# Kernel optimization log

Measured on AMD Instinct MI355X. Metric: run time of the kernel, lower is better.

## Reference

```python
import jax, jax.numpy as jnp
import numpy as np

B, L, E, H = 8, 1024, 512, 8
E2 = 2 * E
EPS = 1e-5


def _spectral_fc(x, w, fw, fb, n):
    # rfft along feature dim, multiply by rfft of learned filter w (1,n), irfft back, then Linear
    xf = jnp.fft.rfft(x, axis=2, norm='ortho')          # [B,L,n//2+1] complex
    wf = jnp.fft.rfft(w, axis=1, norm='ortho')          # [1,n//2+1] complex
    y = jnp.fft.irfft(xf * wf, n=n, axis=2, norm='ortho')
    return y @ fw + fb


def _layernorm(x, g, b):
    m = jnp.mean(x, axis=-1, keepdims=True)
    v = jnp.mean(jnp.square(x - m), axis=-1, keepdims=True)
    return (x - m) * jax.lax.rsqrt(v + EPS) * g + b


def setup_inputs() -> dict:
    key = jax.random.key(0)
    ks = jax.random.split(key, 32)
    s = 0.02

    def lin_w(k, i, o):
        return (jax.random.normal(k, (i, o), jnp.float32) / np.sqrt(i)).astype(jnp.float32)

    def layer_params(k0, k1, n):
        return (s * jax.random.normal(k0, (1, n), jnp.float32), lin_w(k1, n, n), jnp.zeros((n,), jnp.float32))

    attn_w, attn_fw, attn_fb = layer_params(ks[1], ks[2], E)
    ln0_w, ln0_fw, ln0_fb = layer_params(ks[3], ks[4], E)
    ln1_w, ln1_fw, ln1_fb = layer_params(ks[5], ks[6], E)
    ln2_w, ln2_fw, ln2_fb = layer_params(ks[7], ks[8], E)
    ln3_w, ln3_fw, ln3_fb = layer_params(ks[9], ks[10], E2)
    ln4_w, ln4_fw, ln4_fb = layer_params(ks[11], ks[12], E2)

    return {
        'x': jax.random.normal(ks[0], (B, L, E), jnp.float32),
        'attn_w': attn_w, 'attn_fw': attn_fw, 'attn_fb': attn_fb,
        'ln0_w': ln0_w, 'ln0_fw': ln0_fw, 'ln0_fb': ln0_fb,
        'ln1_w': ln1_w, 'ln1_fw': ln1_fw, 'ln1_fb': ln1_fb,
        'ln2_w': ln2_w, 'ln2_fw': ln2_fw, 'ln2_fb': ln2_fb,
        'ln3_w': ln3_w, 'ln3_fw': ln3_fw, 'ln3_fb': ln3_fb,
        'ln4_w': ln4_w, 'ln4_fw': ln4_fw, 'ln4_fb': ln4_fb,
        'n1_g': jnp.ones((E,), jnp.float32), 'n1_b': jnp.zeros((E,), jnp.float32),
        'n2_g': jnp.ones((E,), jnp.float32), 'n2_b': jnp.zeros((E,), jnp.float32),
    }


def reference(x, attn_w, attn_fw, attn_fb,
              ln0_w, ln0_fw, ln0_fb, ln1_w, ln1_fw, ln1_fb,
              ln2_w, ln2_fw, ln2_fb, ln3_w, ln3_fw, ln3_fb,
              ln4_w, ln4_fw, ln4_fb, n1_g, n1_b, n2_g, n2_b):
    q = _spectral_fc(x, attn_w, attn_fw, attn_fb, E).reshape(B, L, H, E // H)
    scores = jnp.einsum('blhe,bshe->bhls', q, q) * (1.0 / np.sqrt(E))
    A = jax.nn.softmax(scores, axis=-1)
    new_x = jnp.einsum('bhls,bshd->blhd', A, q).reshape(B, L, E)

    x1 = _layernorm(x + new_x, n1_g, n1_b)
    x_ln = jax.nn.gelu(_spectral_fc(x1, ln0_w, ln0_fw, ln0_fb, E), approximate=False)
    x2 = x1 - x_ln
    h = jax.nn.sigmoid(_spectral_fc(x2, ln1_w, ln1_fw, ln1_fb, E)) * _spectral_fc(x2, ln2_w, ln2_fw, ln2_fb, E)
    out = jnp.concatenate((new_x, x_ln), axis=-1)  # [B,L,2E]
    out = jax.nn.sigmoid(_spectral_fc(out, ln3_w, ln3_fw, ln3_fb, E2)) * _spectral_fc(out, ln4_w, ln4_fw, ln4_fb, E2)
    return (_layernorm(h, n2_g, n2_b), out)
```

## Files before the change

kernel.cpp:

```cpp
#include <hip/hip_runtime.h>
#include <hip/hip_bf16.h>
#include <math.h>

typedef __hip_bfloat16 bf16;
typedef unsigned short u16;
typedef __attribute__((ext_vector_type(8))) short short8;
typedef __attribute__((ext_vector_type(4))) float f32x4;

#define NB      8
#define SEQ     1024
#define EDIM    512
#define E2DIM   1024
#define ROWS    8192
#define INV_SQRT_E 0.04419417382415922f
#define ATT_SCL    0.06375985678148161f

__device__ inline u16 f2bu(float f) {
    union { float f; unsigned u; } c; c.f = f;
    return (u16)((c.u + 0x7FFF + ((c.u >> 16) & 1)) >> 16);
}

__device__ __forceinline__ unsigned cvtpk_bf16(float lo, float hi) {
    unsigned r;
    asm("v_cvt_pk_bf16_f32 %0, %1, %2" : "=v"(r) : "v"(lo), "v"(hi));
    return r;
}

__global__ __launch_bounds__(256) void detect_dtype(const u16* __restrict__ x,
                                                    int* __restrict__ flag) {
    int t = threadIdx.x;
    int cnt = 0;
    for (int k = t; k < 8192; k += 256) {
        int e = (x[k] >> 7) & 0xFF;
        if (e >= 0xC0) cnt++;
    }
#pragma unroll
    for (int o = 32; o > 0; o >>= 1) cnt += __shfl_xor(cnt, o);
    __shared__ int red[4];
    if ((t & 63) == 0) red[t >> 6] = cnt;
    __syncthreads();
    if (t == 0) flag[0] = (red[0] + red[1] + red[2] + red[3] > 100) ? 1 : 0;
}

struct CvtBatch {
    const void* src[23];
    float4*     dst[23];
    int         pre4[24];
};

__global__ __launch_bounds__(256) void cvt_all(CvtBatch a, int total4,
                                               const int* __restrict__ flag) {
    int t = blockIdx.x * 256 + threadIdx.x;
    if (t >= total4) return;
    int lo = 0;
    while (t >= a.pre4[lo + 1]) lo++;
    int li = t - a.pre4[lo];
    if (flag[0]) {
        a.dst[lo][li] = ((const float4*)a.src[lo])[li];
    } else {
        ushort4 u = ((const ushort4*)a.src[lo])[li];
        union { unsigned int i; float f; } c;
        float4 o;
        c.i = ((unsigned)u.x) << 16; o.x = c.f;
        c.i = ((unsigned)u.y) << 16; o.y = c.f;
        c.i = ((unsigned)u.z) << 16; o.z = c.f;
        c.i = ((unsigned)u.w) << 16; o.w = c.f;
        a.dst[lo][li] = o;
    }
}

__global__ __launch_bounds__(256) void f2b_kernel(const float* __restrict__ src,
                                                  u16* __restrict__ dst, int n4) {
    int i = blockIdx.x * 256 + threadIdx.x;
    if (i >= n4) return;
    float4 a = ((const float4*)src)[i];
    ushort4 o;
    o.x = f2bu(a.x); o.y = f2bu(a.y); o.z = f2bu(a.z); o.w = f2bu(a.w);
    ((ushort4*)dst)[i] = o;
}

#define LDK 32

__device__ __forceinline__ void stage128x32(const u16* g, int ld, u16* lds, int tid) {
    const int w = tid >> 6;
    const int l = tid & 63;
    const int r = w * 16 + (l >> 2);
    const int c = (l & 3) * 8;
    const u16* g0 = g + (size_t)r * ld + c;
    u16* l0 = lds + w * 16 * LDK;
    __builtin_amdgcn_global_load_lds(
        (const __attribute__((address_space(1))) void*)g0,
        (__attribute__((address_space(3))) void*)l0, 16, 0, 0);
    const u16* g1 = g0 + (size_t)64 * ld;
    u16* l1 = l0 + 64 * LDK;
    __builtin_amdgcn_global_load_lds(
        (const __attribute__((address_space(1))) void*)g1,
        (__attribute__((address_space(3))) void*)l1, 16, 0, 0);
}

__device__ __forceinline__ void stage64x32(const u16* g, int ld, u16* lds, int tid) {
    const int w = tid >> 6;
    const int l = tid & 63;
    const int r = w * 16 + (l >> 2);
    const int c = (l & 3) * 8;
    const u16* g0 = g + (size_t)r * ld + c;
    u16* l0 = lds + w * 16 * LDK;
    __builtin_amdgcn_global_load_lds(
        (const __attribute__((address_space(1))) void*)g0,
        (__attribute__((address_space(3))) void*)l0, 16, 0, 0);
}

__device__ __forceinline__ void xcd_swz(int& bx, int& by) {
    const int nx  = gridDim.x;
    const int nwg = nx * gridDim.y;
    const int lid = blockIdx.y * nx + blockIdx.x;
    const int q   = nwg >> 3;
    const int s   = (lid & 7) * q + (lid >> 3);
    bx = s % nx;
    by = s / nx;
}

struct FoldBatch {
    const float* w[6];
    const float* fw[6];
    u16* t1[6];
    u16* t2[6];
    u16* mt[6];
    int  n[6], lg[6];
    float sc[6];
};

__global__ __launch_bounds__(256) void fold_trconv(FoldBatch fb) {
    const int z = blockIdx.z;
    const int n = fb.n[z];
    const int bx = blockIdx.x * 32, by = blockIdx.y * 32;
    if (bx >= n || by >= n) return;
    __shared__ float t[32][33];
    const int tx = threadIdx.x & 31, ty = threadIdx.x >> 5;
    const float* src = fb.fw[z];
    u16* dst = fb.t1[z];
#pragma unroll
    for (int r = 0; r < 32; r += 8)
        t[ty + r][tx] = src[(size_t)(by + ty + r) * n + bx + tx];
    __syncthreads();
#pragma unroll
    for (int r = 0; r < 32; r += 8)
        dst[(size_t)(bx + ty + r) * n + by + tx] = f2bu(t[tx][ty + r]);
}

__global__ __launch_bounds__(256) void fold_circ(FoldBatch fb) {
    const int z = blockIdx.z;
    const int n = fb.n[z], lg = fb.lg[z];
    int idx = blockIdx.x * 256 + threadIdx.x;
    if (idx >= n * n) return;
    int mask = n - 1;
    int m = idx & mask;
    int j = idx >> lg;
    fb.t2[z][idx] = f2bu(fb.w[z][(m - j) & mask]);
}

__global__ __launch_bounds__(256) void fold_gemm(FoldBatch fb) {
    const int z = blockIdx.z;
    const int n = fb.n[z];
    const int bm = blockIdx.y * 128, bn = blockIdx.x * 128;
    if (bm >= n || bn >= n) return;
    const u16* A  = fb.t1[z];
    const u16* Bt = fb.t2[z];
    u16* Mt = fb.mt[z];
    const float scale = fb.sc[z];

    __shared__ u16 Asl[2][128 * LDK];
    __shared__ u16 Bsl[2][128 * LDK];
    const int tid = threadIdx.x;
    const int lane = tid & 63, wave = tid >> 6;
    const int wy = wave >> 1, wx = wave & 1;
    const int qd = lane >> 4, ln16 = lane & 15;

    f32x4 acc[4][4];
#pragma unroll
    for (int i = 0; i < 4; i++)
#pragma unroll
        for (int j = 0; j < 4; j++)
#pragma unroll
            for (int r = 0; r < 4; r++) acc[i][j][r] = 0.f;

    const u16* Ab = A  + (size_t)bm * n;
    const u16* Bb = Bt + (size_t)bn * n;
    stage128x32(Ab, n, Asl[0], tid);
    stage128x32(Bb, n, Bsl[0], tid);
    __syncthreads();
    int cur = 0;
    for (int k0 = 0; k0 < n; k0 += 32) {
        if (k0 + 32 < n) {
            stage128x32(Ab + k0 + 32, n, Asl[cur ^ 1], tid);
            stage128x32(Bb + k0 + 32, n, Bsl[cur ^ 1], tid);
        }
        const u16* Ac = Asl[cur];
        const u16* Bc = Bsl[cur];
        short8 af[4], bf_[4];
#pragma unroll
        for (int i = 0; i < 4; i++) {
            af[i]  = *(const short8*)&Ac[(wy * 64 + i * 16 + ln16) * LDK + qd * 8];
            bf_[i] = *(const short8*)&Bc[(wx * 64 + i * 16 + ln16) * LDK + qd * 8];
        }
#pragma unroll
        for (int i = 0; i < 4; i++)
#pragma unroll
            for (int j = 0; j < 4; j++)
                acc[i][j] = __builtin_amdgcn_mfma_f32_16x16x32_bf16(af[i], bf_[j], acc[i][j], 0, 0, 0);
        __syncthreads();
        cur ^= 1;
    }
#pragma unroll
    for (int i = 0; i < 4; i++)
#pragma unroll
        for (int j = 0; j < 4; j++) {
            const int col = bn + wx * 64 + j * 16 + ln16;
#pragma unroll
            for (int r = 0; r < 4; r++) {
                const int row = bm + wy * 64 + i * 16 + qd * 4 + r;
                Mt[(size_t)row * n + col] = f2bu(acc[i][j][r] * scale);
            }
        }
}

__global__ __launch_bounds__(256) void gemm_bf(
    const u16* __restrict__ A, int lda,
    const u16* __restrict__ Bt, int ldb,
    const float* __restrict__ bias,
    float* __restrict__ Cf, int ldc,
    u16* __restrict__ Cb, int ldcb,
    u16* __restrict__ Cb2, int ldcb2,
    const float* __restrict__ aux, int ldaux,
    int K, int mode)
{
    __shared__ u16 Asl[2][128 * LDK];
    __shared__ u16 Bsl[2][64 * LDK];
    const int tid = threadIdx.x;
    int bxs, bys;
    xcd_swz(bxs, bys);
    const int bm = bys * 128, bn = bxs * 64;
    const int lane = tid & 63, wave = tid >> 6;
    const int wy = wave >> 1, wx = wave & 1;
    const int qd = lane >> 4, ln16 = lane & 15;

    f32x4 acc[4][2];
#pragma unroll
    for (int i = 0; i < 4; i++)
#pragma unroll
        for (int j = 0; j < 2; j++)
#pragma unroll
            for (int r = 0; r < 4; r++) acc[i][j][r] = 0.f;

    const u16* Ab = A  + (size_t)bm * lda;
    const u16* Bb = Bt + (size_t)bn * ldb;
    stage128x32(Ab, lda, Asl[0], tid);
    stage64x32(Bb, ldb, Bsl[0], tid);
    __syncthreads();
    int cur = 0;
    for (int k0 = 0; k0 < K; k0 += 32) {
        if (k0 + 32 < K) {
            stage128x32(Ab + k0 + 32, lda, Asl[cur ^ 1], tid);
            stage64x32(Bb + k0 + 32, ldb, Bsl[cur ^ 1], tid);
        }
        const u16* Ac = Asl[cur];
        const u16* Bc = Bsl[cur];
        short8 af[4], bf_[2];
#pragma unroll
        for (int i = 0; i < 4; i++)
            af[i]  = *(const short8*)&Ac[(wy * 64 + i * 16 + ln16) * LDK + qd * 8];
#pragma unroll
        for (int j = 0; j < 2; j++)
            bf_[j] = *(const short8*)&Bc[(wx * 32 + j * 16 + ln16) * LDK + qd * 8];
#pragma unroll
        for (int i = 0; i < 4; i++)
#pragma unroll
            for (int j = 0; j < 2; j++)
                acc[i][j] = __builtin_amdgcn_mfma_f32_16x16x32_bf16(af[i], bf_[j], acc[i][j], 0, 0, 0);
        __syncthreads();
        cur ^= 1;
    }

#pragma unroll
    for (int i = 0; i < 4; i++) {
#pragma unroll
        for (int j = 0; j < 2; j++) {
            const int col = bn + wx * 32 + j * 16 + ln16;
            const float b_ = bias ? bias[col] : 0.f;
#pragma unroll
            for (int r = 0; r < 4; r++) {
                const int row = bm + wy * 64 + i * 16 + qd * 4 + r;
                float v = acc[i][j][r] + b_;
                if (mode == 1) v = 0.5f * v * (1.0f + erff(v * 0.7071067811865476f));
                if (Cf)  Cf[(size_t)row * ldc + col] = v;
                if (Cb)  Cb[(size_t)row * ldcb + col] = f2bu(v);
                if (Cb2) Cb2[(size_t)row * ldcb2 + col] =
                             f2bu(aux[(size_t)row * ldaux + col] - v);
            }
        }
    }
}

__global__ __launch_bounds__(256) void gemm_bf2(
    const u16* __restrict__ A, int lda,
    const u16* __restrict__ B1t, const u16* __restrict__ B2t, int ldb,
    const float* __restrict__ bias1, const float* __restrict__ bias2,
    float* __restrict__ Cf, int ldc, int K)
{
    __shared__ u16 Asl[2][128 * LDK];
    __shared__ u16 B1sl[2][64 * LDK];
    __shared__ u16 B2sl[2][64 * LDK];
    const int tid = threadIdx.x;
    int bxs, bys;
    xcd_swz(bxs, bys);
    const int bm = bys * 128, bn = bxs * 64;
    const int lane = tid & 63, wave = tid >> 6;
    const int wy = wave >> 1, wx = wave & 1;
    const int qd = lane >> 4, ln16 = lane & 15;

    f32x4 acc1[4][2], acc2[4][2];
#pragma unroll
    for (int i = 0; i < 4; i++)
#pragma unroll
        for (int j = 0; j < 2; j++)
#pragma unroll
            for (int r = 0; r < 4; r++) { acc1[i][j][r] = 0.f; acc2[i][j][r] = 0.f; }

    const u16* Ab  = A   + (size_t)bm * lda;
    const u16* B1b = B1t + (size_t)bn * ldb;
    const u16* B2b = B2t + (size_t)bn * ldb;
    stage128x32(Ab,  lda, Asl[0],  tid);
    stage64x32(B1b, ldb, B1sl[0], tid);
    stage64x32(B2b, ldb, B2sl[0], tid);
    __syncthreads();
    int cur = 0;
    for (int k0 = 0; k0 < K; k0 += 32) {
        if (k0 + 32 < K) {
            stage128x32(Ab  + k0 + 32, lda, Asl[cur ^ 1],  tid);
            stage64x32(B1b + k0 + 32, ldb, B1sl[cur ^ 1], tid);
            stage64x32(B2b + k0 + 32, ldb, B2sl[cur ^ 1], tid);
        }
        const u16* Ac  = Asl[cur];
        const u16* B1c = B1sl[cur];
        const u16* B2c = B2sl[cur];
        short8 af[4], b1f[2], b2f[2];
#pragma unroll
        for (int i = 0; i < 4; i++)
            af[i]  = *(const short8*)&Ac [(wy * 64 + i * 16 + ln16) * LDK + qd * 8];
#pragma unroll
        for (int j = 0; j < 2; j++) {
            b1f[j] = *(const short8*)&B1c[(wx * 32 + j * 16 + ln16) * LDK + qd * 8];
            b2f[j] = *(const short8*)&B2c[(wx * 32 + j * 16 + ln16) * LDK + qd * 8];
        }
#pragma unroll
        for (int i = 0; i < 4; i++)
#pragma unroll
            for (int j = 0; j < 2; j++) {
                acc1[i][j] = __builtin_amdgcn_mfma_f32_16x16x32_bf16(af[i], b1f[j], acc1[i][j], 0, 0, 0);
                acc2[i][j] = __builtin_amdgcn_mfma_f32_16x16x32_bf16(af[i], b2f[j], acc2[i][j], 0, 0, 0);
            }
        __syncthreads();
        cur ^= 1;
    }

#pragma unroll
    for (int i = 0; i < 4; i++) {
#pragma unroll
        for (int j = 0; j < 2; j++) {
            const int col = bn + wx * 32 + j * 16 + ln16;
            const float b1_ = bias1[col], b2_ = bias2[col];
#pragma unroll
            for (int r = 0; r < 4; r++) {
                const int row = bm + wy * 64 + i * 16 + qd * 4 + r;
                const float g = 1.0f / (1.0f + expf(-(acc1[i][j][r] + b1_)));
                Cf[(size_t)row * ldc + col] = g * (acc2[i][j][r] + b2_);
            }
        }
    }
}

__global__ __launch_bounds__(256) void ln_kernel(
    const float* __restrict__ in0, int ld0,
    const u16* __restrict__ in1b, int ld1b,
    const float* __restrict__ g, const float* __restrict__ bta,
    float* __restrict__ outf, int ldo,
    u16* __restrict__ outb, int ldob)
{
    int row = blockIdx.x, tid = threadIdx.x;
    const float* p0 = in0 + (size_t)row * ld0;
    float v0 = p0[tid], v1 = p0[tid + 256];
    if (in1b) {
        const u16* p1 = in1b + (size_t)row * ld1b;
        union { unsigned u; float f; } c0, c1;
        c0.u = ((unsigned)p1[tid]) << 16;
        c1.u = ((unsigned)p1[tid + 256]) << 16;
        v0 += c0.f; v1 += c1.f;
    }
    float s = v0 + v1, sq = v0 * v0 + v1 * v1;
#pragma unroll
    for (int o = 32; o > 0; o >>= 1) {
        s  += __shfl_xor(s, o);
        sq += __shfl_xor(sq, o);
    }
    __shared__ float red[8];
    int wid = tid >> 6;
    if ((tid & 63) == 0) { red[wid] = s; red[4 + wid] = sq; }
    __syncthreads();
    s  = red[0] + red[1] + red[2] + red[3];
    sq = red[4] + red[5] + red[6] + red[7];
    float mean = s * (1.0f / 512.0f);
    float var  = sq * (1.0f / 512.0f) - mean * mean;
    float rstd = rsqrtf(var + 1e-5f);
    float o0 = (v0 - mean) * rstd * g[tid] + bta[tid];
    float o1 = (v1 - mean) * rstd * g[tid + 256] + bta[tid + 256];
    if (outf) {
        outf[(size_t)row * ldo + tid]       = o0;
        outf[(size_t)row * ldo + tid + 256] = o1;
    }
    if (outb) {
        outb[(size_t)row * ldob + tid]       = f2bu(o0);
        outb[(size_t)row * ldob + tid + 256] = f2bu(o1);
    }
}

#define AP 80

__global__ __launch_bounds__(256) void attn_mfma(const u16* __restrict__ qall,
                                                 u16* __restrict__ catb) {
    __shared__ u16 Ks[64 * AP];
    __shared__ u16 KsT[64 * AP];
    __shared__ u16 Pw[4][16 * AP];

    const int bid = blockIdx.x;
    const int lt = bid & 15, hh = (bid >> 4) & 7, bb = bid >> 7;
    const int q0 = lt * 64;
    const int tid = threadIdx.x;
    const int wave = tid >> 6, lane = tid & 63;
    const int quad = lane >> 4, ln16 = lane & 15;

    const u16* qh = qall + (size_t)bb * SEQ * EDIM + hh * 64;

    const u16* qrow = qh + (size_t)(q0 + wave * 16 + ln16) * EDIM + quad * 8;
    const short8 aq0 = *(const short8*)(qrow);
    const short8 aq1 = *(const short8*)(qrow + 32);

    f32x4 oacc[4];
    float m_run = -1e30f, l_run = 0.f;
#pragma unroll
    for (int j = 0; j < 4; j++)
#pragma unroll
        for (int r = 0; r < 4; r++) oacc[j][r] = 0.f;

    const int sr  = tid & 63;
    const int scq = (tid >> 6) * 16;

    for (int s0 = 0; s0 < SEQ; s0 += 64) {
        __syncthreads();
        {
            const u16* krow = qh + (size_t)(s0 + sr) * EDIM + scq;
            uint4 v0 = *(const uint4*)(krow);
            uint4 v1 = *(const uint4*)(krow + 8);
            *(uint4*)&Ks[sr * AP + scq]     = v0;
            *(uint4*)&Ks[sr * AP + scq + 8] = v1;
            const u16* h0 = (const u16*)&v0;
            const u16* h1 = (const u16*)&v1;
#pragma unroll
            for (int i = 0; i < 8; i++) KsT[(scq + i) * AP + sr]     = h0[i];
#pragma unroll
            for (int i = 0; i < 8; i++) KsT[(scq + 8 + i) * AP + sr] = h1[i];
        }
        __syncthreads();

        f32x4 S[4];
#pragma unroll
        for (int j = 0; j < 4; j++) {
            const int krw = (j * 16 + ln16) * AP + quad * 8;
            short8 a0 = *(const short8*)&Ks[krw];
            short8 a1 = *(const short8*)&Ks[krw + 32];
            f32x4 c = {0.f, 0.f, 0.f, 0.f};
            c = __builtin_amdgcn_mfma_f32_16x16x32_bf16(a0, aq0, c, 0, 0, 0);
            c = __builtin_amdgcn_mfma_f32_16x16x32_bf16(a1, aq1, c, 0, 0, 0);
            S[j] = c;
        }

        float mx = S[0][0];
#pragma unroll
        for (int j = 0; j < 4; j++)
#pragma unroll
            for (int r = 0; r < 4; r++) mx = fmaxf(mx, S[j][r]);
        mx = fmaxf(mx, __shfl_xor(mx, 16));
        mx = fmaxf(mx, __shfl_xor(mx, 32));
        const float mn = fmaxf(m_run, mx);
        const float al = exp2f((m_run - mn) * ATT_SCL);
        m_run = mn;
        const float ns = -mn * ATT_SCL;
        float p[4][4];
        float rs = 0.f;
#pragma unroll
        for (int j = 0; j < 4; j++)
#pragma unroll
            for (int r = 0; r < 4; r++) {
                p[j][r] = exp2f(fmaf(S[j][r], ATT_SCL, ns));
                rs += p[j][r];
            }
        rs += __shfl_xor(rs, 16);
        rs += __shfl_xor(rs, 32);
        l_run = l_run * al + rs;

#pragma unroll
        for (int j = 0; j < 4; j++) {
            unsigned w0 = cvtpk_bf16(p[j][0], p[j][1]);
            unsigned w1 = cvtpk_bf16(p[j][2], p[j][3]);
            *(uint2*)&Pw[wave][ln16 * AP + j * 16 + quad * 4] = make_uint2(w0, w1);
        }

        float alq[4];
#pragma unroll
        for (int r = 0; r < 4; r++) alq[r] = __shfl(al, quad * 4 + r);
#pragma unroll
        for (int j = 0; j < 4; j++)
#pragma unroll
            for (int r = 0; r < 4; r++) oacc[j][r] *= alq[r];

        short8 pa0 = *(const short8*)&Pw[wave][ln16 * AP + quad * 8];
        short8 pa1 = *(const short8*)&Pw[wave][ln16 * AP + 32 + quad * 8];

#pragma unroll
        for (int j = 0; j < 4; j++) {
            const int drw = (j * 16 + ln16) * AP + quad * 8;
            short8 b0 = *(const short8*)&KsT[drw];
            short8 b1 = *(const short8*)&KsT[drw + 32];
            oacc[j] = __builtin_amdgcn_mfma_f32_16x16x32_bf16(pa0, b0, oacc[j], 0, 0, 0);
            oacc[j] = __builtin_amdgcn_mfma_f32_16x16x32_bf16(pa1, b1, oacc[j], 0, 0, 0);
        }
    }

    const float linv = 1.0f / l_run;
    float invq[4];
#pragma unroll
    for (int r = 0; r < 4; r++) invq[r] = __shfl(linv, quad * 4 + r);
#pragma unroll
    for (int r = 0; r < 4; r++) {
        const int row = bb * SEQ + q0 + wave * 16 + quad * 4 + r;
#pragma unroll
        for (int j = 0; j < 4; j++) {
            const int col = hh * 64 + j * 16 + ln16;
            catb[(size_t)row * E2DIM + col] = f2bu(oacc[j][r] * invq[r]);
        }
    }
}

extern "C" void kernel_launch(void* const* d_in, const int* in_sizes, int n_in,
                              void* d_out, int out_size, void* d_ws, size_t ws_size,
                              hipStream_t stream)
{
    const size_t OFF_MT0 = 0;
    const size_t OFF_MT1 = OFF_MT0 + 131072;
    const size_t OFF_MT2 = OFF_MT1 + 131072;
    const size_t OFF_MT3 = OFF_MT2 + 131072;
    const size_t OFF_MT4 = OFF_MT3 + 131072;
    const size_t OFF_MT5 = OFF_MT4 + 524288;
    const size_t OFF_XB  = OFF_MT5 + 524288;
    const size_t OFF_CB  = OFF_XB + 2097152;
    const size_t OFF_BQ  = OFF_CB + 4194304;
    const size_t OFF_BN  = OFF_BQ + 4194304;
    const size_t OFF_BC  = OFF_BN + 4194304;
    const size_t OFF_P   = OFF_BC + 4194304;

    float* W = (float*)d_ws;
    u16* MT[6] = {(u16*)(W + OFF_MT0), (u16*)(W + OFF_MT1), (u16*)(W + OFF_MT2),
                  (u16*)(W + OFF_MT3), (u16*)(W + OFF_MT4), (u16*)(W + OFF_MT5)};
    u16*   XB  = (u16*)(W + OFF_XB);
    u16*   CB  = (u16*)(W + OFF_CB);
    u16*   QB  = (u16*)(W + OFF_BQ);
    float* BN  = W + OFF_BN;
    float* BC  = W + OFF_BC;

    float* F[23];
    CvtBatch cb;
    int pre = 0;
    for (int i = 0; i < 23 && i < n_in; i++) {
        cb.pre4[i] = pre;
        F[i] = W + OFF_P + (size_t)pre * 4;
        cb.src[i] = d_in[i];
        cb.dst[i] = (float4*)F[i];
        pre += in_sizes[i] / 4;
    }
    cb.pre4[23] = pre;
    const int total4 = pre;
    int* FLAG = (int*)(W + OFF_P + (size_t)total4 * 4);

    if (n_in < 23) return;
    if (ws_size < (OFF_P + (size_t)total4 * 4 + 16) * sizeof(float)) return;

    detect_dtype<<<1, 256, 0, stream>>>((const u16*)d_in[0], FLAG);
    cvt_all<<<(total4 + 255) / 256, 256, 0, stream>>>(cb, total4, FLAG);
    f2b_kernel<<<(ROWS * EDIM / 4 + 255) / 256, 256, 0, stream>>>(F[0], XB, ROWS * EDIM / 4);

    FoldBatch fb;
    {
        const int wi[6] = {1, 4, 7, 10, 13, 16};
        u16* T1 = (u16*)BN;
        u16* T2 = (u16*)BC;
        size_t off = 0;
        for (int s = 0; s < 6; s++) {
            const int n = (s < 4) ? 512 : 1024;
            fb.w[s]  = F[wi[s]];
            fb.fw[s] = F[wi[s] + 1];
            fb.t1[s] = T1 + off;
            fb.t2[s] = T2 + off;
            fb.mt[s] = MT[s];
            fb.n[s]  = n;
            fb.lg[s] = (s < 4) ? 9 : 10;
            fb.sc[s] = (s < 4) ? 0.04419417382415922f : 0.03125f;
            off += (size_t)n * n;
        }
    }
    fold_trconv<<<dim3(32, 32, 6), 256, 0, stream>>>(fb);
    fold_circ<<<dim3(4096, 1, 6), 256, 0, stream>>>(fb);
    fold_gemm<<<dim3(8, 8, 6), 256, 0, stream>>>(fb);

    float* out0 = (float*)d_out;
    float* out1 = (float*)d_out + (size_t)ROWS * EDIM;

    gemm_bf<<<dim3(8, 64), 256, 0, stream>>>(
        XB, 512, MT[0], 512, F[3], nullptr, 0, QB, 512, nullptr, 0, nullptr, 0, 512, 0);
    attn_mfma<<<1024, 256, 0, stream>>>(QB, CB);
    ln_kernel<<<8192, 256, 0, stream>>>(F[0], 512, CB, 1024, F[19], F[20],
                                        BC, 512, XB, 512);
    gemm_bf<<<dim3(8, 64), 256, 0, stream>>>(
        XB, 512, MT[1], 512, F[6], nullptr, 0, CB + 512, 1024, QB, 512, BC, 512, 512, 1);
    gemm_bf2<<<dim3(8, 64), 256, 0, stream>>>(
        QB, 512, MT[2], MT[3], 512, F[9], F[12], BN, 512, 512);
    ln_kernel<<<8192, 256, 0, stream>>>(BN, 512, nullptr, 0, F[21], F[22],
                                        out0, 512, nullptr, 0);
    gemm_bf2<<<dim3(16, 64), 256, 0, stream>>>(
        CB, 1024, MT[4], MT[5], 1024, F[15], F[18], out1, 1024, 1024);
}
```

Baseline: 348.4 us.

## Deepen GEMM load pipeline with vmcnt waits and early buffer refill

Restructures the k-loop of three GEMM kernels so two tiles are in flight. Each iteration waits with a partial vmcnt only for the current tile, reads its fragments, then issues the load for tile t+2 into the buffer just freed before running the MFMAs. A peeled final iteration drains the pipeline. This aims to hide global-load latency behind compute and drop one full __syncthreads per iteration, but it depends on stage helpers issuing exactly the assumed number of load instructions (4 or 3) for the vmcnt counts to stay correct.

```diff
diff --git a/kernel.cpp b/kernel.cpp
--- a/kernel.cpp
+++ b/kernel.cpp
@@ -25,6 +25,18 @@
     asm("v_cvt_pk_bf16_f32 %0, %1, %2" : "=v"(r) : "v"(lo), "v"(hi));
     return r;
 }
+
+#define VMCNT(N) do { \
+    asm volatile("s_waitcnt vmcnt(" #N ")" ::: "memory"); \
+    __builtin_amdgcn_sched_barrier(0); \
+    __builtin_amdgcn_s_barrier(); \
+    __builtin_amdgcn_sched_barrier(0); } while (0)
+
+#define LGKM0_BAR() do { \
+    asm volatile("s_waitcnt lgkmcnt(0)" ::: "memory"); \
+    __builtin_amdgcn_sched_barrier(0); \
+    __builtin_amdgcn_s_barrier(); \
+    __builtin_amdgcn_sched_barrier(0); } while (0)
 
 __global__ __launch_bounds__(256) void detect_dtype(const u16* __restrict__ x,
                                                     int* __restrict__ flag) {
@@ -186,15 +198,14 @@
 
     const u16* Ab = A  + (size_t)bm * n;
     const u16* Bb = Bt + (size_t)bn * n;
+    const int nt = n >> 5;
     stage128x32(Ab, n, Asl[0], tid);
     stage128x32(Bb, n, Bsl[0], tid);
-    __syncthreads();
+    stage128x32(Ab + 32, n, Asl[1], tid);
+    stage128x32(Bb + 32, n, Bsl[1], tid);
     int cur = 0;
-    for (int k0 = 0; k0 < n; k0 += 32) {
-        if (k0 + 32 < n) {
-            stage128x32(Ab + k0 + 32, n, Asl[cur ^ 1], tid);
-            stage128x32(Bb + k0 + 32, n, Bsl[cur ^ 1], tid);
-        }
+    for (int t = 0; t < nt - 1; ++t) {
+        VMCNT(4);
         const u16* Ac = Asl[cur];
         const u16* Bc = Bsl[cur];
         short8 af[4], bf_[4];
@@ -203,13 +214,34 @@
             af[i]  = *(const short8*)&Ac[(wy * 64 + i * 16 + ln16) * LDK + qd * 8];
             bf_[i] = *(const short8*)&Bc[(wx * 64 + i * 16 + ln16) * LDK + qd * 8];
         }
+        LGKM0_BAR();
+        if (t + 2 < nt) {
+            const int k2 = (t + 2) * 32;
+            stage128x32(Ab + k2, n, Asl[cur], tid);
+            stage128x32(Bb + k2, n, Bsl[cur], tid);
+        }
 #pragma unroll
         for (int i = 0; i < 4; i++)
 #pragma unroll
             for (int j = 0; j < 4; j++)
                 acc[i][j] = __builtin_amdgcn_mfma_f32_16x16x32_bf16(af[i], bf_[j], acc[i][j], 0, 0, 0);
-        __syncthreads();
         cur ^= 1;
+    }
+    VMCNT(0);
+    {
+        const u16* Ac = Asl[cur];
+        const u16* Bc = Bsl[cur];
+        short8 af[4], bf_[4];
+#pragma unroll
+        for (int i = 0; i < 4; i++) {
+            af[i]  = *(const short8*)&Ac[(wy * 64 + i * 16 + ln16) * LDK + qd * 8];
+            bf_[i] = *(const short8*)&Bc[(wx * 64 + i * 16 + ln16) * LDK + qd * 8];
+        }
+#pragma unroll
+        for (int i = 0; i < 4; i++)
+#pragma unroll
+            for (int j = 0; j < 4; j++)
+                acc[i][j] = __builtin_amdgcn_mfma_f32_16x16x32_bf16(af[i], bf_[j], acc[i][j], 0, 0, 0);
     }
 #pragma unroll
     for (int i = 0; i < 4; i++)
@@ -254,15 +286,14 @@
 
     const u16* Ab = A  + (size_t)bm * lda;
     const u16* Bb = Bt + (size_t)bn * ldb;
+    const int nt = K >> 5;
     stage128x32(Ab, lda, Asl[0], tid);
     stage64x32(Bb, ldb, Bsl[0], tid);
-    __syncthreads();
+    stage128x32(Ab + 32, lda, Asl[1], tid);
+    stage64x32(Bb + 32, ldb, Bsl[1], tid);
     int cur = 0;
-    for (int k0 = 0; k0 < K; k0 += 32) {
-        if (k0 + 32 < K) {
-            stage128x32(Ab + k0 + 32, lda, Asl[cur ^ 1], tid);
-            stage64x32(Bb + k0 + 32, ldb, Bsl[cur ^ 1], tid);
-        }
+    for (int t = 0; t < nt - 1; ++t) {
+        VMCNT(3);
         const u16* Ac = Asl[cur];
         const u16* Bc = Bsl[cur];
         short8 af[4], bf_[2];
@@ -272,13 +303,35 @@
 #pragma unroll
         for (int j = 0; j < 2; j++)
             bf_[j] = *(const short8*)&Bc[(wx * 32 + j * 16 + ln16) * LDK + qd * 8];
+        LGKM0_BAR();
+        if (t + 2 < nt) {
+            const int k2 = (t + 2) * 32;
+            stage128x32(Ab + k2, lda, Asl[cur], tid);
+            stage64x32(Bb + k2, ldb, Bsl[cur], tid);
+        }
 #pragma unroll
         for (int i = 0; i < 4; i++)
 #pragma unroll
             for (int j = 0; j < 2; j++)
                 acc[i][j] = __builtin_amdgcn_mfma_f32_16x16x32_bf16(af[i], bf_[j], acc[i][j], 0, 0, 0);
-        __syncthreads();
         cur ^= 1;
+    }
+    VMCNT(0);
+    {
+        const u16* Ac = Asl[cur];
+        const u16* Bc = Bsl[cur];
+        short8 af[4], bf_[2];
+#pragma unroll
+        for (int i = 0; i < 4; i++)
+            af[i]  = *(const short8*)&Ac[(wy * 64 + i * 16 + ln16) * LDK + qd * 8];
+#pragma unroll
+        for (int j = 0; j < 2; j++)
+            bf_[j] = *(const short8*)&Bc[(wx * 32 + j * 16 + ln16) * LDK + qd * 8];
+#pragma unroll
+        for (int i = 0; i < 4; i++)
+#pragma unroll
+            for (int j = 0; j < 2; j++)
+                acc[i][j] = __builtin_amdgcn_mfma_f32_16x16x32_bf16(af[i], bf_[j], acc[i][j], 0, 0, 0);
     }
 
 #pragma unroll
@@ -329,17 +382,16 @@
     const u16* Ab  = A   + (size_t)bm * lda;
     const u16* B1b = B1t + (size_t)bn * ldb;
     const u16* B2b = B2t + (size_t)bn * ldb;
+    const int nt = K >> 5;
     stage128x32(Ab,  lda, Asl[0],  tid);
     stage64x32(B1b, ldb, B1sl[0], tid);
     stage64x32(B2b, ldb, B2sl[0], tid);
-    __syncthreads();
+    stage128x32(Ab + 32,  lda, Asl[1],  tid);
+    stage64x32(B1b + 32, ldb, B1sl[1], tid);
+    stage64x32(B2b + 32, ldb, B2sl[1], tid);
     int cur = 0;
-    for (int k0 = 0; k0 < K; k0 += 32) {
-        if (k0 + 32 < K) {
-            stage128x32(Ab  + k0 + 32, lda, Asl[cur ^ 1],  tid);
-            stage64x32(B1b + k0 + 32, ldb, B1sl[cur ^ 1], tid);
-            stage64x32(B2b + k0 + 32, ldb, B2sl[cur ^ 1], tid);
-        }
+    for (int t = 0; t < nt - 1; ++t) {
+        VMCNT(4);
         const u16* Ac  = Asl[cur];
         const u16* B1c = B1sl[cur];
         const u16* B2c = B2sl[cur];
@@ -352,6 +404,13 @@
             b1f[j] = *(const short8*)&B1c[(wx * 32 + j * 16 + ln16) * LDK + qd * 8];
             b2f[j] = *(const short8*)&B2c[(wx * 32 + j * 16 + ln16) * LDK + qd * 8];
         }
+        LGKM0_BAR();
+        if (t + 2 < nt) {
+            const int k2 = (t + 2) * 32;
+            stage128x32(Ab  + k2, lda, Asl[cur],  tid);
+            stage64x32(B1b + k2, ldb, B1sl[cur], tid);
+            stage64x32(B2b + k2, ldb, B2sl[cur], tid);
+        }
 #pragma unroll
         for (int i = 0; i < 4; i++)
 #pragma unroll
@@ -359,8 +418,29 @@
                 acc1[i][j] = __builtin_amdgcn_mfma_f32_16x16x32_bf16(af[i], b1f[j], acc1[i][j], 0, 0, 0);
                 acc2[i][j] = __builtin_amdgcn_mfma_f32_16x16x32_bf16(af[i], b2f[j], acc2[i][j], 0, 0, 0);
             }
-        __syncthreads();
         cur ^= 1;
+    }
+    VMCNT(0);
+    {
+        const u16* Ac  = Asl[cur];
+        const u16* B1c = B1sl[cur];
+        const u16* B2c = B2sl[cur];
+        short8 af[4], b1f[2], b2f[2];
+#pragma unroll
+        for (int i = 0; i < 4; i++)
+            af[i]  = *(const short8*)&Ac [(wy * 64 + i * 16 + ln16) * LDK + qd * 8];
+#pragma unroll
+        for (int j = 0; j < 2; j++) {
+            b1f[j] = *(const short8*)&B1c[(wx * 32 + j * 16 + ln16) * LDK + qd * 8];
+            b2f[j] = *(const short8*)&B2c[(wx * 32 + j * 16 + ln16) * LDK + qd * 8];
+        }
+#pragma unroll
+        for (int i = 0; i < 4; i++)
+#pragma unroll
+            for (int j = 0; j < 2; j++) {
+                acc1[i][j] = __builtin_amdgcn_mfma_f32_16x16x32_bf16(af[i], b1f[j], acc1[i][j], 0, 0, 0);
+                acc2[i][j] = __builtin_amdgcn_mfma_f32_16x16x32_bf16(af[i], b2f[j], acc2[i][j], 0, 0, 0);
+            }
     }
 
 #pragma unroll
```

After: 334.4 us. -4.0%, faster.
